# Optimization experiments

Measured on AMD Instinct MI355X. Metric: run time of the kernel, lower is better.

Reference implementation:

```python
import jax, jax.numpy as jnp
import numpy as np

N = 4096          # number_of_node
DIN = 3           # dim_input (forced: fc1 expects N*dim_input == N*3 after last stage)
DOUT = 4          # dim_output
DACT = N          # dim_action defaults to number_of_node
B = 128


def setup_inputs() -> dict:
    key = jax.random.key(0)
    ks = jax.random.split(key, 12)
    X = jax.random.normal(ks[0], (B, N * DIN), dtype=jnp.float32)
    adj = jax.random.uniform(ks[1], (N, N), dtype=jnp.float32)
    def lin(kw, kb, fan_in, fan_out):
        bound = 1.0 / np.sqrt(fan_in)
        W = jax.random.uniform(kw, (fan_in, fan_out), minval=-bound, maxval=bound, dtype=jnp.float32)
        b = jax.random.uniform(kb, (fan_out,), minval=-bound, maxval=bound, dtype=jnp.float32)
        return W, b
    W1, b1 = lin(ks[2], ks[3], DIN, 4)
    W2, b2 = lin(ks[4], ks[5], 4, DOUT)
    W3, b3 = lin(ks[6], ks[7], DOUT, 3)
    Wfc, bfc = lin(ks[8], ks[9], N * DIN, 54)
    Wout, bout = lin(ks[10], ks[11], 54, DACT)
    return {"X": X, "adj": adj, "W1": W1, "b1": b1, "W2": W2, "b2": b2,
            "W3": W3, "b3": b3, "Wfc": Wfc, "bfc": bfc, "Wout": Wout, "bout": bout}


def reference(X, adj, W1, b1, W2, b2, W3, b3, Wfc, bfc, Wout, bout):
    # X: [B, N*DIN] -> [B, N, DIN]
    h = X.reshape(X.shape[0], N, DIN)
    # three (adj @ h) aggregations fused with tiny Linear + ReLU
    h = jax.nn.relu(jnp.einsum('nm,bmf->bnf', adj, h) @ W1 + b1)   # [B,N,4]
    h = jax.nn.relu(jnp.einsum('nm,bmf->bnf', adj, h) @ W2 + b2)   # [B,N,DOUT]
    h = jax.nn.relu(jnp.einsum('nm,bmf->bnf', adj, h) @ W3 + b3)   # [B,N,3]
    flat = h.reshape(h.shape[0], -1)                               # [B, N*3]
    hid = jax.nn.relu(flat @ Wfc + bfc)                            # [B, 54]
    q_value = hid @ Wout + bout                                    # [B, DACT]
    return q_value
```

## Files before the change

kernel.cpp:

```cpp
#include <hip/hip_runtime.h>


typedef __bf16 bf16x8 __attribute__((ext_vector_type(8)));
typedef float  f32x4  __attribute__((ext_vector_type(4)));

#define N_NODE 4096
#define BATCH  128

__global__ __launch_bounds__(256) void prep_k(const float* __restrict__ adj,
                                              __bf16* __restrict__ adjB,
                                              const float* __restrict__ X,
                                              const float* __restrict__ W1,
                                              __bf16* __restrict__ G0,
                                              float* __restrict__ hid_acc) {
    const int blk = blockIdx.x, tx = threadIdx.x;
    if (blk < 8192) {
        const int g = blk * 256 + tx;
        const int lane = g & 63, ka = (g >> 6) & 127, rb = g >> 13;
        const int row = rb * 16 + (lane & 15);
        const int kb  = ka * 32 + ((lane >> 4) & 3) * 8;
        const float4* s = (const float4*)(adj + (size_t)row * 4096 + kb);
        float4 u = s[0];
        float4 v = s[1];
        bf16x8 o = { (__bf16)u.x, (__bf16)u.y, (__bf16)u.z, (__bf16)u.w,
                     (__bf16)v.x, (__bf16)v.y, (__bf16)v.z, (__bf16)v.w };
        *(bf16x8*)(adjB + (size_t)g * 8) = o;
    } else if (blk < 9216) {
        const int g = (blk - 8192) * 256 + tx;
        const int lp = g & 63, cbg = (g >> 6) & 31, kc = g >> 11;
        const int c = cbg * 16 + (lp & 15);
        const int b = c >> 2, f = c & 3;
        const float w0 = W1[0 * 4 + f], w1 = W1[1 * 4 + f], w2 = W1[2 * 4 + f];
        const int mb = kc * 32 + ((lp >> 4) & 3) * 8;
        const float* Xb = X + (size_t)b * 12288 + (size_t)mb * 3;
        bf16x8 o;
#pragma unroll
        for (int j = 0; j < 8; ++j) {
            const float v = Xb[j * 3 + 0] * w0 + Xb[j * 3 + 1] * w1 + Xb[j * 3 + 2] * w2;
            o[j] = (__bf16)v;
        }
        *(bf16x8*)(G0 + (size_t)g * 8) = o;
    } else {
        const int i = (blk - 9216) * 256 + tx;
        if (i < BATCH * 54) hid_acc[i] = 0.f;
    }
}

template <int MODE>
__global__ __launch_bounds__(256, 2) void gcn_k(const __bf16* __restrict__ A,
                                                const __bf16* __restrict__ Bp,
                                                const float* __restrict__ Wa,
                                                const float* __restrict__ ba,
                                                const float* __restrict__ Wb,
                                                __bf16* __restrict__ Op,
                                                float* __restrict__ H3out) {
    __shared__ __align__(16) unsigned char smem[50688];
    const int tx = threadIdx.x;
    const int wk = tx >> 6, lane = tx & 63;
    const int quad = lane >> 4, lr = lane & 15;

    const int l = blockIdx.x;
    const int xcd = l & 7, s = l >> 3;
    const int mi = xcd * 8 + (s & 7), ci = s >> 3;
    const int m0 = mi * 64, c0 = ci * 64;

    const __bf16* pA[4];
#pragma unroll
    for (int i = 0; i < 4; ++i)
        pA[i] = A + (size_t)(mi * 4 + i) * 65536 + wk * 512 + lane * 8;
    const __bf16* pB[4];
#pragma unroll
    for (int j = 0; j < 4; ++j)
        pB[j] = Bp + (size_t)(wk * 32 + ci * 4 + j) * 512 + lane * 8;

    f32x4 acc[4][4] = {};

#pragma unroll 4
    for (int kt = 0; kt < 32; ++kt) {
        bf16x8 af[4], bv[4];
#pragma unroll
        for (int i = 0; i < 4; ++i)
            af[i] = *(const bf16x8*)(pA[i] + kt * 2048);
#pragma unroll
        for (int j = 0; j < 4; ++j)
            bv[j] = *(const bf16x8*)(pB[j] + kt * 65536);
#pragma unroll
        for (int i = 0; i < 4; ++i)
#pragma unroll
            for (int j = 0; j < 4; ++j)
                acc[i][j] = __builtin_amdgcn_mfma_f32_16x16x32_bf16(
                    af[i], bv[j], acc[i][j], 0, 0, 0);
    }

    __syncthreads();
    float* part = (float*)smem;
    const int sb = (wk >> 1) * 4096;
    if (wk & 1) {
#pragma unroll
        for (int t = 0; t < 16; ++t)
            *(f32x4*)(part + sb + t * 256 + lane * 4) = acc[t >> 2][t & 3];
    }
    __syncthreads();
    if (!(wk & 1)) {
#pragma unroll
        for (int t = 0; t < 16; ++t)
            acc[t >> 2][t & 3] += *(const f32x4*)(part + sb + t * 256 + lane * 4);
    }
    __syncthreads();
    if (wk == 2) {
#pragma unroll
        for (int t = 0; t < 16; ++t)
            *(f32x4*)(part + t * 256 + lane * 4) = acc[t >> 2][t & 3];
    }
    __syncthreads();
    float* Ct = (float*)(smem + 32768);
    if (wk == 0) {
#pragma unroll
        for (int t = 0; t < 16; ++t)
            acc[t >> 2][t & 3] += *(const f32x4*)(part + t * 256 + lane * 4);
#pragma unroll
        for (int i = 0; i < 4; ++i)
#pragma unroll
            for (int j = 0; j < 4; ++j)
#pragma unroll
                for (int r = 0; r < 4; ++r)
                    Ct[(i * 16 + quad * 4 + r) * 66 + j * 16 + lr] = acc[i][j][r];
    }
    __syncthreads();

    if (MODE == 0) {
#pragma unroll
        for (int it = 0; it < 2; ++it) {
            const int g = it * 256 + tx;
            const int lp = g & 63, cbl = (g >> 6) & 3, kcl = g >> 8;
            const int cl = cbl * 16 + (lp & 15);
            const float bf = ba[cl & 3];
            const int mb = kcl * 32 + ((lp >> 4) & 3) * 8;
            bf16x8 o;
#pragma unroll
            for (int j = 0; j < 8; ++j)
                o[j] = (__bf16)fmaxf(Ct[(mb + j) * 66 + cl] + bf, 0.f);
            *(bf16x8*)(Op + ((size_t)((mi * 2 + kcl) * 32 + (ci * 4 + cbl)) * 64 + lp) * 8) = o;
        }
    } else if (MODE == 1) {
        float W2l[16], W3l[12], bl2[4];
#pragma unroll
        for (int i = 0; i < 16; ++i) W2l[i] = Wa[i];
#pragma unroll
        for (int i = 0; i < 12; ++i) W3l[i] = Wb[i];
#pragma unroll
        for (int i = 0; i < 4; ++i) bl2[i] = ba[i];
#pragma unroll
        for (int it = 0; it < 2; ++it) {
            const int g = it * 256 + tx;
            const int lp = g & 63, cbl = (g >> 6) & 3, kcl = g >> 8;
            const int cl = cbl * 16 + (lp & 15);
            const int bloc = cl >> 2, f3 = cl & 3;
            const int mb = kcl * 32 + ((lp >> 4) & 3) * 8;
            bf16x8 o;
#pragma unroll
            for (int j = 0; j < 8; ++j) {
                const float* row = &Ct[(mb + j) * 66 + bloc * 4];
                float v = 0.f;
                if (f3 < 3) {
#pragma unroll
                    for (int fo = 0; fo < 4; ++fo) {
                        const float tmp = fmaxf(row[0] * W2l[fo] + row[1] * W2l[4 + fo] +
                                                row[2] * W2l[8 + fo] + row[3] * W2l[12 + fo] +
                                                bl2[fo], 0.f);
                        const float w3a = W3l[fo * 3 + 0], w3b = W3l[fo * 3 + 1],
                                    w3c = W3l[fo * 3 + 2];
                        v += tmp * (f3 == 0 ? w3a : (f3 == 1 ? w3b : w3c));
                    }
                }
                o[j] = (__bf16)v;
            }
            *(bf16x8*)(Op + ((size_t)((mi * 2 + kcl) * 32 + (ci * 4 + cbl)) * 64 + lp) * 8) = o;
        }
    } else {
        const int m_l = tx & 63, cq = tx >> 6;
#pragma unroll
        for (int t = 0; t < 16; ++t) {
            const int cl = cq * 16 + t;
            const int c = c0 + cl, b = c >> 2, f = c & 3;
            if (f < 3)
                H3out[(size_t)(b * 3 + f) * N_NODE + m0 + m_l] =
                    fmaxf(Ct[m_l * 66 + cl] + ba[f], 0.f);
        }
    }
}

__global__ __launch_bounds__(256) void fc1p_k(const float* __restrict__ H3,
                                              const float* __restrict__ Wfc,
                                              float* __restrict__ hid_acc) {
    __shared__ float hs[16 * 192];
    __shared__ float red[4][16][64];
    const int tx = threadIdx.x;
    const int wv = tx >> 6, lane = tx & 63;
    const int n0 = blockIdx.x * 64;
    const int b0 = blockIdx.y * 16;

    for (int idx = tx; idx < 3072; idx += 256) {
        const int n = idx & 63, f = (idx >> 6) % 3, b = idx / 192;
        hs[idx] = H3[((size_t)((b0 + b) * 3 + f)) * N_NODE + n0 + n];
    }
    __syncthreads();

    float acc[16];
#pragma unroll
    for (int b = 0; b < 16; ++b) acc[b] = 0.f;
    if (lane < 54) {
        const int nb = wv * 16;
        for (int n = 0; n < 16; ++n) {
#pragma unroll
            for (int f = 0; f < 3; ++f) {
                const float w = Wfc[((size_t)(n0 + nb + n) * 3 + f) * 54 + lane];
#pragma unroll
                for (int b = 0; b < 16; ++b)
                    acc[b] += hs[b * 192 + f * 64 + nb + n] * w;
            }
        }
    }
#pragma unroll
    for (int b = 0; b < 16; ++b) red[wv][b][lane] = acc[b];
    __syncthreads();
    if (wv == 0 && lane < 54) {
        for (int b = 0; b < 16; ++b) {
            const float s = red[0][b][lane] + red[1][b][lane] +
                            red[2][b][lane] + red[3][b][lane];
            atomicAdd(&hid_acc[(b0 + b) * 54 + lane], s);
        }
    }
}

__global__ __launch_bounds__(256) void fc2_k(const float* __restrict__ hid_acc,
                                             const float* __restrict__ bfc,
                                             const float* __restrict__ Wout,
                                             const float* __restrict__ bout,
                                             float* __restrict__ out) {
    const int tx = threadIdx.x;
    const int a  = blockIdx.x * 256 + tx;
    const int b0 = blockIdx.y * 4;
    __shared__ float hs[4 * 54];
    if (tx < 216) {
        const int j = tx % 54;
        hs[tx] = fmaxf(hid_acc[b0 * 54 + tx] + bfc[j], 0.f);
    }
    __syncthreads();
    float a0 = 0.f, a1 = 0.f, a2 = 0.f, a3 = 0.f;
    for (int j = 0; j < 54; ++j) {
        float w = Wout[(size_t)j * N_NODE + a];
        a0 += hs[0 * 54 + j] * w;
        a1 += hs[1 * 54 + j] * w;
        a2 += hs[2 * 54 + j] * w;
        a3 += hs[3 * 54 + j] * w;
    }
    float bo = bout[a];
    out[(size_t)(b0 + 0) * N_NODE + a] = a0 + bo;
    out[(size_t)(b0 + 1) * N_NODE + a] = a1 + bo;
    out[(size_t)(b0 + 2) * N_NODE + a] = a2 + bo;
    out[(size_t)(b0 + 3) * N_NODE + a] = a3 + bo;
}

extern "C" void kernel_launch(void* const* d_in, const int* in_sizes, int n_in,
                              void* d_out, int out_size, void* d_ws, size_t ws_size,
                              hipStream_t stream) {
    const float* X    = (const float*)d_in[0];
    const float* adj  = (const float*)d_in[1];
    const float* W1   = (const float*)d_in[2];
    const float* b1   = (const float*)d_in[3];
    const float* W2   = (const float*)d_in[4];
    const float* b2   = (const float*)d_in[5];
    const float* W3   = (const float*)d_in[6];
    const float* b3   = (const float*)d_in[7];
    const float* Wfc  = (const float*)d_in[8];
    const float* bfc  = (const float*)d_in[9];
    const float* Wout = (const float*)d_in[10];
    const float* bout = (const float*)d_in[11];
    float* out = (float*)d_out;

    char* w = (char*)d_ws;
    __bf16* adjB = (__bf16*)w;
    __bf16* G0   = (__bf16*)(w + 33554432);
    __bf16* H1   = (__bf16*)(w + 33554432 + 4194304);
    __bf16* H2g  = (__bf16*)(w + 33554432 + 2 * 4194304);
    float*  H3   = (float*)(w + 33554432 + 3 * 4194304);
    float*  hid  = (float*)(w + 33554432 + 3 * 4194304 + 6291456);

    prep_k<<<9243, 256, 0, stream>>>(adj, adjB, X, W1, G0, hid);

    gcn_k<0><<<512, 256, 0, stream>>>(adjB, G0, nullptr, b1, nullptr, H1, nullptr);
    gcn_k<1><<<512, 256, 0, stream>>>(adjB, H1, W2, b2, W3, H2g, nullptr);
    gcn_k<2><<<512, 256, 0, stream>>>(adjB, H2g, nullptr, b3, nullptr, nullptr, H3);

    fc1p_k<<<dim3(64, 8), 256, 0, stream>>>(H3, Wfc, hid);
    fc2_k<<<dim3(16, 32), 256, 0, stream>>>(hid, bfc, Wout, bout, out);
}
```

Measured before the change: 228.3 us.

## Fuse fc1 into final GCN layer and parallelize split-K reduction

The third GCN kernel now applies bias+ReLU and multiplies directly by Wfc, atomically accumulating into the hidden buffer. This removes the H3 round-trip through global memory and the separate fc1 kernel launch. The cross-wave split-K reduction is also restructured: all four waves write partials, then each wave reduces a quarter of the tiles, replacing the serial tree of syncs. LDS use grows to 64KB per block, which could affect occupancy at two blocks per CU.

Result: faster. 218.4 us (-4.3%).

```diff
diff --git a/kernel.cpp b/kernel.cpp
--- a/kernel.cpp
+++ b/kernel.cpp
@@ -53,8 +53,8 @@
                                                 const float* __restrict__ ba,
                                                 const float* __restrict__ Wb,
                                                 __bf16* __restrict__ Op,
-                                                float* __restrict__ H3out) {
-    __shared__ __align__(16) unsigned char smem[50688];
+                                                float* __restrict__ hidOut) {
+    __shared__ __align__(16) unsigned char smem[65536];
     const int tx = threadIdx.x;
     const int wk = tx >> 6, lane = tx & 63;
     const int quad = lane >> 4, lr = lane & 15;
@@ -62,7 +62,7 @@
     const int l = blockIdx.x;
     const int xcd = l & 7, s = l >> 3;
     const int mi = xcd * 8 + (s & 7), ci = s >> 3;
-    const int m0 = mi * 64, c0 = ci * 64;
+    const int m0 = mi * 64;
 
     const __bf16* pA[4];
 #pragma unroll
@@ -92,40 +92,28 @@
                     af[i], bv[j], acc[i][j], 0, 0, 0);
     }
 
-    __syncthreads();
     float* part = (float*)smem;
-    const int sb = (wk >> 1) * 4096;
-    if (wk & 1) {
-#pragma unroll
-        for (int t = 0; t < 16; ++t)
-            *(f32x4*)(part + sb + t * 256 + lane * 4) = acc[t >> 2][t & 3];
-    }
-    __syncthreads();
-    if (!(wk & 1)) {
-#pragma unroll
-        for (int t = 0; t < 16; ++t)
-            acc[t >> 2][t & 3] += *(const f32x4*)(part + sb + t * 256 + lane * 4);
-    }
-    __syncthreads();
-    if (wk == 2) {
-#pragma unroll
-        for (int t = 0; t < 16; ++t)
-            *(f32x4*)(part + t * 256 + lane * 4) = acc[t >> 2][t & 3];
-    }
-    __syncthreads();
-    float* Ct = (float*)(smem + 32768);
-    if (wk == 0) {
-#pragma unroll
-        for (int t = 0; t < 16; ++t)
-            acc[t >> 2][t & 3] += *(const f32x4*)(part + t * 256 + lane * 4);
-#pragma unroll
-        for (int i = 0; i < 4; ++i)
-#pragma unroll
-            for (int j = 0; j < 4; ++j)
-#pragma unroll
-                for (int r = 0; r < 4; ++r)
-                    Ct[(i * 16 + quad * 4 + r) * 66 + j * 16 + lr] = acc[i][j][r];
-    }
+#pragma unroll
+    for (int t = 0; t < 16; ++t)
+        *(f32x4*)(part + wk * 4096 + t * 256 + lane * 4) = acc[t >> 2][t & 3];
+    __syncthreads();
+    f32x4 fin[4];
+#pragma unroll
+    for (int u = 0; u < 4; ++u) {
+        const int t = wk * 4 + u;
+        f32x4 s0 = *(const f32x4*)(part + 0     + t * 256 + lane * 4);
+        f32x4 s1 = *(const f32x4*)(part + 4096  + t * 256 + lane * 4);
+        f32x4 s2 = *(const f32x4*)(part + 8192  + t * 256 + lane * 4);
+        f32x4 s3 = *(const f32x4*)(part + 12288 + t * 256 + lane * 4);
+        fin[u] = (s0 + s1) + (s2 + s3);
+    }
+    __syncthreads();
+    float* Ct = (float*)smem;
+#pragma unroll
+    for (int u = 0; u < 4; ++u)
+#pragma unroll
+        for (int r = 0; r < 4; ++r)
+            Ct[(wk * 16 + quad * 4 + r) * 66 + u * 16 + lr] = fin[u][r];
     __syncthreads();
 
     if (MODE == 0) {
@@ -178,57 +166,35 @@
             *(bf16x8*)(Op + ((size_t)((mi * 2 + kcl) * 32 + (ci * 4 + cbl)) * 64 + lp) * 8) = o;
         }
     } else {
-        const int m_l = tx & 63, cq = tx >> 6;
-#pragma unroll
-        for (int t = 0; t < 16; ++t) {
-            const int cl = cq * 16 + t;
-            const int c = c0 + cl, b = c >> 2, f = c & 3;
-            if (f < 3)
-                H3out[(size_t)(b * 3 + f) * N_NODE + m0 + m_l] =
-                    fmaxf(Ct[m_l * 66 + cl] + ba[f], 0.f);
-        }
-    }
-}
-
-__global__ __launch_bounds__(256) void fc1p_k(const float* __restrict__ H3,
-                                              const float* __restrict__ Wfc,
-                                              float* __restrict__ hid_acc) {
-    __shared__ float hs[16 * 192];
-    __shared__ float red[4][16][64];
-    const int tx = threadIdx.x;
-    const int wv = tx >> 6, lane = tx & 63;
-    const int n0 = blockIdx.x * 64;
-    const int b0 = blockIdx.y * 16;
-
-    for (int idx = tx; idx < 3072; idx += 256) {
-        const int n = idx & 63, f = (idx >> 6) % 3, b = idx / 192;
-        hs[idx] = H3[((size_t)((b0 + b) * 3 + f)) * N_NODE + n0 + n];
-    }
-    __syncthreads();
-
-    float acc[16];
-#pragma unroll
-    for (int b = 0; b < 16; ++b) acc[b] = 0.f;
-    if (lane < 54) {
-        const int nb = wv * 16;
-        for (int n = 0; n < 16; ++n) {
-#pragma unroll
-            for (int f = 0; f < 3; ++f) {
-                const float w = Wfc[((size_t)(n0 + nb + n) * 3 + f) * 54 + lane];
-#pragma unroll
-                for (int b = 0; b < 16; ++b)
-                    acc[b] += hs[b * 192 + f * 64 + nb + n] * w;
+        float* red = (float*)(smem + 17408);
+        const float b30 = ba[0], b31 = ba[1], b32 = ba[2];
+        float accf[16];
+#pragma unroll
+        for (int b = 0; b < 16; ++b) accf[b] = 0.f;
+        if (lane < 54) {
+            for (int nn = 0; nn < 16; ++nn) {
+                const int n = wk * 16 + nn;
+#pragma unroll
+                for (int f = 0; f < 3; ++f) {
+                    const float w = Wa[((size_t)(m0 + n) * 3 + f) * 54 + lane];
+                    const float bf = (f == 0) ? b30 : (f == 1 ? b31 : b32);
+#pragma unroll
+                    for (int b = 0; b < 16; ++b) {
+                        const float r = fmaxf(Ct[n * 66 + b * 4 + f] + bf, 0.f);
+                        accf[b] += r * w;
+                    }
+                }
             }
         }
-    }
-#pragma unroll
-    for (int b = 0; b < 16; ++b) red[wv][b][lane] = acc[b];
-    __syncthreads();
-    if (wv == 0 && lane < 54) {
-        for (int b = 0; b < 16; ++b) {
-            const float s = red[0][b][lane] + red[1][b][lane] +
-                            red[2][b][lane] + red[3][b][lane];
-            atomicAdd(&hid_acc[(b0 + b) * 54 + lane], s);
+#pragma unroll
+        for (int b = 0; b < 16; ++b) red[(wk * 16 + b) * 64 + lane] = accf[b];
+        __syncthreads();
+        if (wk == 0 && lane < 54) {
+            for (int b = 0; b < 16; ++b) {
+                const float s2 = red[b * 64 + lane] + red[(16 + b) * 64 + lane] +
+                                 red[(32 + b) * 64 + lane] + red[(48 + b) * 64 + lane];
+                atomicAdd(&hidOut[(ci * 16 + b) * 54 + lane], s2);
+            }
         }
     }
 }
@@ -284,15 +250,13 @@
     __bf16* G0   = (__bf16*)(w + 33554432);
     __bf16* H1   = (__bf16*)(w + 33554432 + 4194304);
     __bf16* H2g  = (__bf16*)(w + 33554432 + 2 * 4194304);
-    float*  H3   = (float*)(w + 33554432 + 3 * 4194304);
-    float*  hid  = (float*)(w + 33554432 + 3 * 4194304 + 6291456);
+    float*  hid  = (float*)(w + 33554432 + 3 * 4194304);
 
     prep_k<<<9243, 256, 0, stream>>>(adj, adjB, X, W1, G0, hid);
 
     gcn_k<0><<<512, 256, 0, stream>>>(adjB, G0, nullptr, b1, nullptr, H1, nullptr);
     gcn_k<1><<<512, 256, 0, stream>>>(adjB, H1, W2, b2, W3, H2g, nullptr);
-    gcn_k<2><<<512, 256, 0, stream>>>(adjB, H2g, nullptr, b3, nullptr, nullptr, H3);
-
-    fc1p_k<<<dim3(64, 8), 256, 0, stream>>>(H3, Wfc, hid);
+    gcn_k<2><<<512, 256, 0, stream>>>(adjB, H2g, Wfc, b3, nullptr, nullptr, hid);
+
     fc2_k<<<dim3(16, 32), 256, 0, stream>>>(hid, bfc, Wout, bout, out);
 }
```
